# Performance work log

Hardware: AMD Instinct MI355X
Metric: run time of the kernel (lower is better)

Reference implementation:

```python
import jax, jax.numpy as jnp
import numpy as np

B, P, S, D, H = 4, 256, 4096, 1024, 16
HD = D // H
EPS = 1e-5


def setup_inputs() -> dict:
    key = jax.random.key(0)
    ks = jax.random.split(key, 12)
    patch_embeddings = jax.random.normal(ks[0], (B, P, D), dtype=jnp.float32)
    byte_hidden_states = jax.random.normal(ks[1], (B, S, D), dtype=jnp.float32)
    # contiguous non-overlapping spans of 16 bytes per patch
    starts = jnp.broadcast_to(jnp.arange(P, dtype=jnp.int64) * (S // P), (B, P))
    ends = starts + (S // P)
    patch_positions = jnp.stack([starts, ends], axis=-1)  # (B, P, 2)
    byte_mask = jnp.ones((B, S), dtype=jnp.float32)
    scale = 0.02
    return {
        "patch_embeddings": patch_embeddings,
        "byte_hidden_states": byte_hidden_states,
        "patch_positions": patch_positions,
        "byte_mask": byte_mask,
        "ln_gamma": jnp.ones((D,), jnp.float32),
        "ln_beta": jnp.zeros((D,), jnp.float32),
        "w_q": jax.random.normal(ks[2], (D, D), jnp.float32) * scale,
        "b_q": jnp.zeros((D,), jnp.float32),
        "w_k": jax.random.normal(ks[3], (D, D), jnp.float32) * scale,
        "b_k": jnp.zeros((D,), jnp.float32),
        "w_v": jax.random.normal(ks[4], (D, D), jnp.float32) * scale,
        "b_v": jnp.zeros((D,), jnp.float32),
        "w_o": jax.random.normal(ks[5], (D, D), jnp.float32) * scale,
        "b_o": jnp.zeros((D,), jnp.float32),
    }


def _layernorm(x, gamma, beta):
    mu = jnp.mean(x, axis=-1, keepdims=True)
    var = jnp.mean(jnp.square(x - mu), axis=-1, keepdims=True)
    return (x - mu) * jax.lax.rsqrt(var + EPS) * gamma + beta


def reference(patch_embeddings, byte_hidden_states, patch_positions, byte_mask,
              ln_gamma, ln_beta, w_q, b_q, w_k, b_k, w_v, b_v, w_o, b_o):
    b, p, d = patch_embeddings.shape
    s = byte_hidden_states.shape[1]
    h, hd = H, d // H

    start = patch_positions[..., 0]  # (B,P)
    end = patch_positions[..., 1]
    idx = jnp.arange(s)
    valid_span = (start < s) & (end <= s) & (start < end)  # (B,P)
    window = (idx[None, None, :] >= start[..., None]) & (idx[None, None, :] < end[..., None])
    allowed = window & valid_span[..., None]               # (B,P,S) boolean mask
    allowed = allowed & (byte_mask[:, None, :] != 0.0)

    # query from layernormed patch embeddings (1 query per patch)
    qx = _layernorm(patch_embeddings, ln_gamma, ln_beta)
    q = (qx @ w_q.T + b_q).reshape(b, p, h, hd)
    k = (byte_hidden_states @ w_k.T + b_k).reshape(b, s, h, hd)
    v = (byte_hidden_states @ w_v.T + b_v).reshape(b, s, h, hd)

    scale = 1.0 / jnp.sqrt(jnp.asarray(hd, patch_embeddings.dtype))
    scores = jnp.einsum('bphd,bshd->bhps', q, k) * scale      # (B,H,P,S)
    scores = jnp.where(allowed[:, None, :, :], scores, jnp.asarray(-1e9, scores.dtype))
    attn = jax.nn.softmax(scores, axis=-1)
    out = jnp.einsum('bhps,bshd->bphd', attn, v).reshape(b, p, d)
    out = out @ w_o.T + b_o

    # dropout is identity in eval mode; residual add
    return patch_embeddings + out
```

## Files before the change

### kernel.cpp

```cpp
#include <hip/hip_runtime.h>
#include <hip/hip_bf16.h>
#include <stdint.h>

#define B_ 4
#define P_ 256
#define S_ 4096
#define D_ 1024
#define H_ 16
#define HD_ 64

typedef __attribute__((ext_vector_type(8))) short short8;
typedef __attribute__((ext_vector_type(4))) short short4v;
typedef __attribute__((ext_vector_type(2))) short short2v;
typedef __attribute__((ext_vector_type(4))) float f32x4;

__device__ __forceinline__ float b2f(short s) {
  return __uint_as_float(((unsigned)(unsigned short)s) << 16);
}
__device__ __forceinline__ short f2bf(float f) {
  unsigned u = __float_as_uint(f);
  unsigned r = (u + 0x7fffu + ((u >> 16) & 1u)) >> 16;
  return (short)(unsigned short)r;
}

__global__ __launch_bounds__(256) void prep2_kernel(
    const float* __restrict__ pe,
    const float* __restrict__ gamma, const float* __restrict__ beta,
    const float* __restrict__ wq, const float* __restrict__ wk,
    const float* __restrict__ wv, const float* __restrict__ wo,
    short* __restrict__ wqb, short* __restrict__ wvb, short* __restrict__ wob,
    short* __restrict__ wkT, short* __restrict__ qx)
{
  const int bid = blockIdx.x;
  const int tid = threadIdx.x;
  if (bid < 1536) {
    const int wi = bid >> 9;
    const size_t base = (size_t)(bid & 511) * 2048 + (size_t)tid * 8;
    const float* src; short* dst;
    if (wi == 0)      { src = wq; dst = wqb; }
    else if (wi == 1) { src = wv; dst = wvb; }
    else              { src = wo; dst = wob; }
    const float4 f0 = *(const float4*)(src + base);
    const float4 f1 = *(const float4*)(src + base + 4);
    short8 o;
    o[0] = f2bf(f0.x); o[1] = f2bf(f0.y); o[2] = f2bf(f0.z); o[3] = f2bf(f0.w);
    o[4] = f2bf(f1.x); o[5] = f2bf(f1.y); o[6] = f2bf(f1.z); o[7] = f2bf(f1.w);
    *(short8*)(dst + base) = o;
  } else if (bid < 1600) {
    __shared__ short Ts[128][132];
    const int t = bid - 1536;
    const int ti = t >> 3, tj = t & 7;
    #pragma unroll
    for (int j = 0; j < 16; ++j) {
      const int r = j * 8 + (tid >> 5);
      const int c4 = (tid & 31) * 4;
      const float4 v = *(const float4*)(wk + (size_t)(ti * 128 + r) * D_ + tj * 128 + c4);
      short4v o;
      o[0] = f2bf(v.x); o[1] = f2bf(v.y); o[2] = f2bf(v.z); o[3] = f2bf(v.w);
      *(short4v*)(&Ts[r][c4]) = o;
    }
    __syncthreads();
    #pragma unroll
    for (int j = 0; j < 16; ++j) {
      const int c = j * 8 + (tid >> 5);
      const int r4 = (tid & 31) * 4;
      short4v o;
      o[0] = Ts[r4 + 0][c]; o[1] = Ts[r4 + 1][c];
      o[2] = Ts[r4 + 2][c]; o[3] = Ts[r4 + 3][c];
      *(short4v*)(wkT + (size_t)(tj * 128 + c) * D_ + ti * 128 + r4) = o;
    }
  } else {
    const int row = bid - 1600;
    const int c = tid * 4;
    const float4 x = *(const float4*)(pe + (size_t)row * D_ + c);
    float s1 = x.x + x.y + x.z + x.w;
    float s2 = x.x * x.x + x.y * x.y + x.z * x.z + x.w * x.w;
    #pragma unroll
    for (int off = 32; off >= 1; off >>= 1) {
      s1 += __shfl_xor(s1, off, 64);
      s2 += __shfl_xor(s2, off, 64);
    }
    __shared__ float red[8];
    const int wid = tid >> 6, lane = tid & 63;
    if (lane == 0) { red[wid] = s1; red[4 + wid] = s2; }
    __syncthreads();
    s1 = red[0] + red[1] + red[2] + red[3];
    s2 = red[4] + red[5] + red[6] + red[7];
    const float mu = s1 * (1.0f / D_);
    const float var = s2 * (1.0f / D_) - mu * mu;
    const float rs = rsqrtf(var + 1e-5f);
    const float4 g = *(const float4*)(gamma + c);
    const float4 bt = *(const float4*)(beta + c);
    short4v o;
    o[0] = f2bf((x.x - mu) * rs * g.x + bt.x);
    o[1] = f2bf((x.y - mu) * rs * g.y + bt.y);
    o[2] = f2bf((x.z - mu) * rs * g.z + bt.z);
    o[3] = f2bf((x.w - mu) * rs * g.w + bt.w);
    *(short4v*)(qx + (size_t)row * D_ + c) = o;
  }
}

__device__ __forceinline__ void gemm64_core(
    const short* __restrict__ A, const short* __restrict__ W,
    int mt, int nt, int Kd, int lda, int ldb,
    f32x4 acc[2][2], short* As, short* Bs)
{
  const int tid = threadIdx.x;
  const int w = tid >> 6, l = tid & 63;
  const int wr = w >> 1, wc = w & 1;
  const int lr = l & 15, lk = l >> 4;
  (void)l; (void)w;

  for (int kt = 0; kt < Kd; kt += 64) {
    __syncthreads();
    #pragma unroll
    for (int j = 0; j < 2; ++j) {
      const int c = j * 256 + tid;
      const int r = c >> 3;
      const int ce = ((c & 7) ^ (r & 7)) * 8;
      __builtin_amdgcn_global_load_lds(
          (const __attribute__((address_space(1))) void*)(A + (size_t)(mt * 64 + r) * lda + kt + ce),
          (__attribute__((address_space(3))) void*)((char*)As + c * 16), 16, 0, 0);
      __builtin_amdgcn_global_load_lds(
          (const __attribute__((address_space(1))) void*)(W + (size_t)(nt * 64 + r) * ldb + kt + ce),
          (__attribute__((address_space(3))) void*)((char*)Bs + c * 16), 16, 0, 0);
    }
    asm volatile("s_waitcnt vmcnt(0)" ::: "memory");
    __syncthreads();
    #pragma unroll
    for (int ks = 0; ks < 2; ++ks) {
      short8 a[2], bfr[2];
      #pragma unroll
      for (int m = 0; m < 2; ++m) {
        const int row = wr * 32 + m * 16 + lr;
        a[m] = *(const short8*)((char*)As + row * 128 + (((ks * 4 + lk) ^ (row & 7)) * 16));
      }
      #pragma unroll
      for (int n = 0; n < 2; ++n) {
        const int row = wc * 32 + n * 16 + lr;
        bfr[n] = *(const short8*)((char*)Bs + row * 128 + (((ks * 4 + lk) ^ (row & 7)) * 16));
      }
      #pragma unroll
      for (int m = 0; m < 2; ++m)
        #pragma unroll
        for (int n = 0; n < 2; ++n)
          acc[m][n] = __builtin_amdgcn_mfma_f32_16x16x32_bf16(a[m], bfr[n], acc[m][n], 0, 0, 0);
    }
  }
}

__global__ __launch_bounds__(256) void gemm_q64(
    const short* __restrict__ qx, const short* __restrict__ wqb,
    const float* __restrict__ b_q, short* __restrict__ Qo)
{
  __shared__ __align__(16) short As[64 * 64];
  __shared__ __align__(16) short Bs[64 * 64];
  const int bid = blockIdx.x;
  const int u = (bid & 7) * 32 + (bid >> 3);
  const int mt = u >> 4, nt = u & 15;

  f32x4 acc[2][2] = {};
  gemm64_core(qx, wqb, mt, nt, D_, D_, D_, acc, As, Bs);

  const int l = threadIdx.x & 63, w = threadIdx.x >> 6;
  const int wr = w >> 1, wc = w & 1;
  const int lr = l & 15, lk = l >> 4;
  #pragma unroll
  for (int n = 0; n < 2; ++n) {
    const int col = nt * 64 + wc * 32 + n * 16 + lr;
    const float bv = b_q[col];
    #pragma unroll
    for (int m = 0; m < 2; ++m) {
      const int row0 = mt * 64 + wr * 32 + m * 16 + lk * 4;
      #pragma unroll
      for (int i = 0; i < 4; ++i)
        Qo[(size_t)(row0 + i) * D_ + col] = f2bf(acc[m][n][i] + bv);
    }
  }
}

__global__ __launch_bounds__(256) void gemm_qt(
    const short* __restrict__ Qo, const short* __restrict__ wkT,
    short* __restrict__ Qt)
{
  __shared__ __align__(16) short As[128 * 64];
  __shared__ __align__(16) short Bs[128 * 64];
  const int bid = blockIdx.x;
  const int hh = bid >> 6, mt = (bid >> 3) & 7, nt = bid & 7;
  const int tid = threadIdx.x;
  const int wid = tid >> 6, l = tid & 63;
  const int wr = wid >> 1, wc = wid & 1;
  const int lr = l & 15, lk = l >> 4;
  const int sr = l >> 3, scol = (l & 7) * 8;

  #pragma unroll
  for (int j = 0; j < 4; ++j) {
    const int r = (wid * 4 + j) * 8 + sr;
    __builtin_amdgcn_global_load_lds(
        (const __attribute__((address_space(1))) void*)(Qo + (size_t)(mt * 128 + r) * D_ + hh * 64 + scol),
        (__attribute__((address_space(3))) void*)(As + (wid * 4 + j) * 512), 16, 0, 0);
    __builtin_amdgcn_global_load_lds(
        (const __attribute__((address_space(1))) void*)(wkT + (size_t)(nt * 128 + r) * D_ + hh * 64 + scol),
        (__attribute__((address_space(3))) void*)(Bs + (wid * 4 + j) * 512), 16, 0, 0);
  }
  asm volatile("s_waitcnt vmcnt(0)" ::: "memory");
  __syncthreads();

  f32x4 acc[4][4] = {};
  #pragma unroll
  for (int ks = 0; ks < 2; ++ks) {
    short8 a[4], bfr[4];
    #pragma unroll
    for (int m = 0; m < 4; ++m)
      a[m] = *(const short8*)(As + (wr * 64 + m * 16 + lr) * 64 + ks * 32 + lk * 8);
    #pragma unroll
    for (int n = 0; n < 4; ++n)
      bfr[n] = *(const short8*)(Bs + (wc * 64 + n * 16 + lr) * 64 + ks * 32 + lk * 8);
    #pragma unroll
    for (int m = 0; m < 4; ++m)
      #pragma unroll
      for (int n = 0; n < 4; ++n)
        acc[m][n] = __builtin_amdgcn_mfma_f32_16x16x32_bf16(a[m], bfr[n], acc[m][n], 0, 0, 0);
  }

  #pragma unroll
  for (int n = 0; n < 4; ++n) {
    const int col = nt * 128 + wc * 64 + n * 16 + lr;
    #pragma unroll
    for (int m = 0; m < 4; ++m) {
      const int row0 = mt * 128 + wr * 64 + m * 16 + lk * 4;
      #pragma unroll
      for (int i = 0; i < 4; ++i)
        Qt[((size_t)(row0 + i) * 16 + hh) * D_ + col] = f2bf(acc[m][n][i]);
    }
  }
}

__global__ __launch_bounds__(512) void attn2_kernel(
    const short* __restrict__ Qt, const float* __restrict__ X,
    const int* __restrict__ pos, const float* __restrict__ mask,
    short* __restrict__ Xbar)
{
  __shared__ __align__(16) short Xs[16 * 1024];
  __shared__ float attnT[16][16];
  __shared__ float rband[16];
  __shared__ float denL[16];
  __shared__ __align__(16) float red[8][256];

  const int bp = blockIdx.x;
  const int b = bp >> 8;
  const int tid = threadIdx.x;
  const int w = tid >> 6, l = tid & 63;
  const int t_l = l & 15;
  const int lk = l >> 4;
  const int hgrp = lk * 4;

  short8 af[4];
  {
    const short* qb = Qt + ((size_t)bp * 16 + t_l) * D_;
    #pragma unroll
    for (int ks = 0; ks < 4; ++ks)
      af[ks] = *(const short8*)(qb + (w * 4 + ks) * 32 + lk * 8);
  }

  const bool is64 = (pos[1] == 0);
  const int start = is64 ? pos[4 * bp]     : pos[2 * bp];
  const int end   = is64 ? pos[4 * bp + 2] : pos[2 * bp + 1];
  const bool valid = (start < S_) && (end <= S_) && (start < end);
  const int lo = valid ? (start < 0 ? 0 : start) : 0;
  const int hi = valid ? end : 0;

  float xacc[16][2];
  #pragma unroll
  for (int h = 0; h < 16; ++h) { xacc[h][0] = 0.f; xacc[h][1] = 0.f; }
  float m_run[4] = {-3.0e38f, -3.0e38f, -3.0e38f, -3.0e38f};
  float den[4] = {0.f, 0.f, 0.f, 0.f};

  for (int c0 = lo; c0 < hi; c0 += 16) {
    __syncthreads();
    #pragma unroll
    for (int j = 0; j < 16; ++j) {
      int rg = c0 + j; rg = rg < S_ ? rg : S_ - 1;
      const float2 xv = *(const float2*)(X + ((size_t)b * S_ + rg) * D_ + tid * 2);
      short2v o;
      o[0] = f2bf(xv.x); o[1] = f2bf(xv.y);
      *(short2v*)((char*)Xs + j * 2048 + ((tid * 4) ^ ((j & 7) << 4))) = o;
    }
    __syncthreads();

    f32x4 c = {};
    const int rsw = (t_l & 7) << 4;
    #pragma unroll
    for (int ks = 0; ks < 4; ++ks) {
      const int kb = ((w * 4 + ks) * 32 + lk * 8) * 2;
      const short8 x8 = *(const short8*)((char*)Xs + t_l * 2048 + (kb ^ rsw));
      c = __builtin_amdgcn_mfma_f32_16x16x32_bf16(af[ks], x8, c, 0, 0, 0);
    }
    *(f32x4*)&red[w][l * 4] = c;
    __syncthreads();
    f32x4 s = *(const f32x4*)&red[0][l * 4];
    #pragma unroll
    for (int ww = 1; ww < 8; ++ww)
      s = s + *(const f32x4*)&red[ww][l * 4];

    const int tg = c0 + t_l;
    const bool ok = (tg < hi) && (mask[(size_t)b * S_ + tg] != 0.f);
    float wgt[4], rr[4];
    #pragma unroll
    for (int i = 0; i < 4; ++i) {
      const float sc = ok ? s[i] * 0.125f : -3.0e38f;
      float cm = sc;
      cm = fmaxf(cm, __shfl_xor(cm, 1, 64));
      cm = fmaxf(cm, __shfl_xor(cm, 2, 64));
      cm = fmaxf(cm, __shfl_xor(cm, 4, 64));
      cm = fmaxf(cm, __shfl_xor(cm, 8, 64));
      const float nm = fmaxf(m_run[i], cm);
      const float r = __expf(m_run[i] - nm);
      const float wv_ = ok ? __expf(sc - nm) : 0.f;
      float ws = wv_;
      ws += __shfl_xor(ws, 1, 64);
      ws += __shfl_xor(ws, 2, 64);
      ws += __shfl_xor(ws, 4, 64);
      ws += __shfl_xor(ws, 8, 64);
      den[i] = den[i] * r + ws;
      m_run[i] = nm;
      wgt[i] = wv_; rr[i] = r;
    }
    if (w == 0) {
      #pragma unroll
      for (int i = 0; i < 4; ++i) attnT[t_l][hgrp + i] = wgt[i];
      if (t_l == 0) {
        #pragma unroll
        for (int i = 0; i < 4; ++i) rband[hgrp + i] = rr[i];
      }
    }
    __syncthreads();

    #pragma unroll
    for (int h = 0; h < 16; ++h) {
      const float rb = rband[h];
      xacc[h][0] *= rb; xacc[h][1] *= rb;
    }
    #pragma unroll
    for (int t = 0; t < 16; ++t) {
      const f32x4 a0 = *(const f32x4*)&attnT[t][0];
      const f32x4 a1 = *(const f32x4*)&attnT[t][4];
      const f32x4 a2 = *(const f32x4*)&attnT[t][8];
      const f32x4 a3 = *(const f32x4*)&attnT[t][12];
      const short2v xv = *(const short2v*)((char*)Xs + t * 2048 + ((tid * 4) ^ ((t & 7) << 4)));
      const float x0 = b2f(xv[0]), x1 = b2f(xv[1]);
      #pragma unroll
      for (int i = 0; i < 4; ++i) {
        xacc[i][0]      += a0[i] * x0; xacc[i][1]      += a0[i] * x1;
        xacc[i + 4][0]  += a1[i] * x0; xacc[i + 4][1]  += a1[i] * x1;
        xacc[i + 8][0]  += a2[i] * x0; xacc[i + 8][1]  += a2[i] * x1;
        xacc[i + 12][0] += a3[i] * x0; xacc[i + 12][1] += a3[i] * x1;
      }
    }
  }

  if (w == 0 && t_l == 0) {
    #pragma unroll
    for (int i = 0; i < 4; ++i) denL[hgrp + i] = den[i];
  }
  __syncthreads();

  bool need = false;
  #pragma unroll
  for (int h = 0; h < 16; ++h) need = need || (denL[h] <= 0.f);
  float ms[2] = {0.f, 0.f};
  if (need) {
    for (int t = 0; t < S_; ++t) {
      const float2 xv = *(const float2*)(X + ((size_t)b * S_ + t) * D_ + tid * 2);
      ms[0] += xv.x; ms[1] += xv.y;
    }
    ms[0] *= (1.f / S_); ms[1] *= (1.f / S_);
  }
  #pragma unroll
  for (int h = 0; h < 16; ++h) {
    const float dL = denL[h];
    short2v o;
    if (dL > 0.f) {
      const float inv = 1.f / dL;
      o[0] = f2bf(xacc[h][0] * inv); o[1] = f2bf(xacc[h][1] * inv);
    } else {
      o[0] = f2bf(ms[0]); o[1] = f2bf(ms[1]);
    }
    *(short2v*)(Xbar + ((size_t)bp * 16 + h) * D_ + tid * 2) = o;
  }
}

__global__ __launch_bounds__(256) void gemm_v64(
    const short* __restrict__ Xbar, const short* __restrict__ wvb,
    const float* __restrict__ b_v, short* __restrict__ AO)
{
  __shared__ __align__(16) short As[64 * 64];
  __shared__ __align__(16) short Bs[64 * 64];
  const int bid = blockIdx.x;
  const int u = (bid & 7) * 32 + (bid >> 3);
  const int h = u >> 4, mt = u & 15;

  f32x4 acc[2][2] = {};
  gemm64_core(Xbar + (size_t)h * D_, wvb + (size_t)h * 64 * D_,
              mt, 0, D_, 16 * D_, D_, acc, As, Bs);

  const int l = threadIdx.x & 63, w = threadIdx.x >> 6;
  const int wr = w >> 1, wc = w & 1;
  const int lr = l & 15, lk = l >> 4;
  #pragma unroll
  for (int n = 0; n < 2; ++n) {
    const int gcol = h * 64 + wc * 32 + n * 16 + lr;
    const float bv = b_v[gcol];
    #pragma unroll
    for (int m = 0; m < 2; ++m) {
      const int row0 = mt * 64 + wr * 32 + m * 16 + lk * 4;
      #pragma unroll
      for (int i = 0; i < 4; ++i)
        AO[(size_t)(row0 + i) * D_ + gcol] = f2bf(acc[m][n][i] + bv);
    }
  }
}

__global__ __launch_bounds__(256) void gemm_o64(
    const short* __restrict__ AO, const short* __restrict__ wob,
    const float* __restrict__ b_o, const float* __restrict__ pe,
    float* __restrict__ out)
{
  __shared__ __align__(16) short As[64 * 64];
  __shared__ __align__(16) short Bs[64 * 64];
  const int bid = blockIdx.x;
  const int u = (bid & 7) * 32 + (bid >> 3);
  const int mt = u >> 4, nt = u & 15;

  f32x4 acc[2][2] = {};
  gemm64_core(AO, wob, mt, nt, D_, D_, D_, acc, As, Bs);

  const int l = threadIdx.x & 63, w = threadIdx.x >> 6;
  const int wr = w >> 1, wc = w & 1;
  const int lr = l & 15, lk = l >> 4;
  #pragma unroll
  for (int n = 0; n < 2; ++n) {
    const int col = nt * 64 + wc * 32 + n * 16 + lr;
    const float bv = b_o[col];
    #pragma unroll
    for (int m = 0; m < 2; ++m) {
      const int row0 = mt * 64 + wr * 32 + m * 16 + lk * 4;
      #pragma unroll
      for (int i = 0; i < 4; ++i) {
        const size_t idx = (size_t)(row0 + i) * D_ + col;
        out[idx] = acc[m][n][i] + bv + pe[idx];
      }
    }
  }
}

extern "C" void kernel_launch(void* const* d_in, const int* in_sizes, int n_in,
                              void* d_out, int out_size, void* d_ws, size_t ws_size,
                              hipStream_t stream)
{
  const float* pe    = (const float*)d_in[0];
  const float* xby   = (const float*)d_in[1];
  const int*   pos   = (const int*)d_in[2];
  const float* mask  = (const float*)d_in[3];
  const float* gamma = (const float*)d_in[4];
  const float* beta  = (const float*)d_in[5];
  const float* w_q   = (const float*)d_in[6];
  const float* b_q   = (const float*)d_in[7];
  const float* w_k   = (const float*)d_in[8];
  const float* b_k   = (const float*)d_in[9];  (void)b_k;
  const float* w_v   = (const float*)d_in[10];
  const float* b_v   = (const float*)d_in[11];
  const float* w_o   = (const float*)d_in[12];
  const float* b_o   = (const float*)d_in[13];

  char* ws = (char*)d_ws;
  short* Qt   = (short*)(ws);
  short* Xbar = (short*)(ws + 33554432);
  short* wqb  = (short*)(ws + 67108864);
  short* wvb  = (short*)(ws + 69206016);
  short* wob  = (short*)(ws + 71303168);
  short* wkT  = (short*)(ws + 73400320);
  short* qx   = (short*)(ws + 75497472);
  short* Qo   = (short*)(ws + 77594624);
  short* AO   = (short*)(ws + 79691776);
  (void)in_sizes; (void)n_in; (void)out_size; (void)ws_size;

  prep2_kernel<<<2624, 256, 0, stream>>>(pe, gamma, beta, w_q, w_k, w_v, w_o,
                                         wqb, wvb, wob, wkT, qx);
  gemm_q64<<<256, 256, 0, stream>>>(qx, wqb, b_q, Qo);
  gemm_qt<<<1024, 256, 0, stream>>>(Qo, wkT, Qt);
  attn2_kernel<<<1024, 512, 0, stream>>>(Qt, xby, pos, mask, Xbar);
  gemm_v64<<<256, 256, 0, stream>>>(Xbar, wvb, b_v, AO);
  gemm_o64<<<256, 256, 0, stream>>>(AO, wob, b_o, pe, (float*)d_out);
}
```

Baseline: 101.2 us.

## Process four patches per attention block with register-prefetched next span

The attention kernel now handles four consecutive patches per block (256 blocks instead of 1024). While one patch is computed, the next patch's first 16 byte rows and its query fragments are prefetched into registers, then written to shared memory. The aim is to hide global load latency behind compute. In exchange there are fewer blocks to fill the GPU (256 blocks on a 256-CU part), more register pressure from the prefetch buffer, and no effect for spans longer than 16 beyond the first chunk.

```diff
diff --git a/kernel.cpp b/kernel.cpp
--- a/kernel.cpp
+++ b/kernel.cpp
@@ -236,7 +236,7 @@
   }
 }
 
-__global__ __launch_bounds__(512) void attn2_kernel(
+__global__ __launch_bounds__(512) void attn5_kernel(
     const short* __restrict__ Qt, const float* __restrict__ X,
     const int* __restrict__ pos, const float* __restrict__ mask,
     short* __restrict__ Xbar)
@@ -247,147 +247,199 @@
   __shared__ float denL[16];
   __shared__ __align__(16) float red[8][256];
 
-  const int bp = blockIdx.x;
-  const int b = bp >> 8;
+  const int bp0 = blockIdx.x * 4;
+  const int b = bp0 >> 8;
   const int tid = threadIdx.x;
   const int w = tid >> 6, l = tid & 63;
-  const int t_l = l & 15;
-  const int lk = l >> 4;
+  const int t_l = l & 15, lk = l >> 4;
   const int hgrp = lk * 4;
 
-  short8 af[4];
-  {
-    const short* qb = Qt + ((size_t)bp * 16 + t_l) * D_;
-    #pragma unroll
-    for (int ks = 0; ks < 4; ++ks)
-      af[ks] = *(const short8*)(qb + (w * 4 + ks) * 32 + lk * 8);
-  }
-
   const bool is64 = (pos[1] == 0);
-  const int start = is64 ? pos[4 * bp]     : pos[2 * bp];
-  const int end   = is64 ? pos[4 * bp + 2] : pos[2 * bp + 1];
-  const bool valid = (start < S_) && (end <= S_) && (start < end);
-  const int lo = valid ? (start < 0 ? 0 : start) : 0;
-  const int hi = valid ? end : 0;
-
-  float xacc[16][2];
-  #pragma unroll
-  for (int h = 0; h < 16; ++h) { xacc[h][0] = 0.f; xacc[h][1] = 0.f; }
-  float m_run[4] = {-3.0e38f, -3.0e38f, -3.0e38f, -3.0e38f};
-  float den[4] = {0.f, 0.f, 0.f, 0.f};
-
-  for (int c0 = lo; c0 < hi; c0 += 16) {
+  int plo[4], phi[4];
+  #pragma unroll
+  for (int p = 0; p < 4; ++p) {
+    const int bp = bp0 + p;
+    const int st = is64 ? pos[4 * bp]     : pos[2 * bp];
+    const int en = is64 ? pos[4 * bp + 2] : pos[2 * bp + 1];
+    const bool v = (st < S_) && (en <= S_) && (st < en);
+    plo[p] = v ? (st < 0 ? 0 : st) : 0;
+    phi[p] = v ? en : 0;
+  }
+
+  float2 pre[16];
+  auto XPRE = [&](int p) {
+    #pragma unroll
+    for (int j = 0; j < 16; ++j) {
+      int rg = plo[p] + j; rg = rg < S_ ? rg : S_ - 1;
+      pre[j] = *(const float2*)(X + ((size_t)b * S_ + rg) * D_ + tid * 2);
+    }
+  };
+  auto XWRITE = [&]() {
+    #pragma unroll
+    for (int j = 0; j < 16; ++j) {
+      short2v o; o[0] = f2bf(pre[j].x); o[1] = f2bf(pre[j].y);
+      *(short2v*)((char*)Xs + j * 2048 + ((tid * 4) ^ ((j & 7) << 4))) = o;
+    }
+  };
+
+  short8 af0[4], af1[4];
+#define LOADAF(arr, bp_)                                                     \
+  {                                                                          \
+    const short* qb_ = Qt + ((size_t)(bp_) * 16 + t_l) * D_;                 \
+    _Pragma("unroll")                                                        \
+    for (int ks = 0; ks < 4; ++ks)                                           \
+      arr[ks] = *(const short8*)(qb_ + (w * 4 + ks) * 32 + lk * 8);          \
+  }
+
+  auto DO_PATCH = [&](const short8 (&af)[4], int p) {
+    const int lo = plo[p], hi = phi[p];
+    const int bp = bp0 + p;
+    float xacc[16][2];
+    #pragma unroll
+    for (int h = 0; h < 16; ++h) { xacc[h][0] = 0.f; xacc[h][1] = 0.f; }
+    float m_run[4] = {-3.0e38f, -3.0e38f, -3.0e38f, -3.0e38f};
+    float den[4] = {0.f, 0.f, 0.f, 0.f};
+
+    bool first = true;
+    for (int c0 = lo; c0 < hi; c0 += 16) {
+      if (!first) {
+        __syncthreads();
+        #pragma unroll
+        for (int j = 0; j < 16; ++j) {
+          int rg = c0 + j; rg = rg < S_ ? rg : S_ - 1;
+          const float2 xv = *(const float2*)(X + ((size_t)b * S_ + rg) * D_ + tid * 2);
+          short2v o; o[0] = f2bf(xv.x); o[1] = f2bf(xv.y);
+          *(short2v*)((char*)Xs + j * 2048 + ((tid * 4) ^ ((j & 7) << 4))) = o;
+        }
+        __syncthreads();
+      }
+      first = false;
+
+      f32x4 c = {};
+      const int rsw = (t_l & 7) << 4;
+      #pragma unroll
+      for (int ks = 0; ks < 4; ++ks) {
+        const int kb = ((w * 4 + ks) * 32 + lk * 8) * 2;
+        const short8 x8 = *(const short8*)((char*)Xs + t_l * 2048 + (kb ^ rsw));
+        c = __builtin_amdgcn_mfma_f32_16x16x32_bf16(af[ks], x8, c, 0, 0, 0);
+      }
+      *(f32x4*)&red[w][l * 4] = c;
+      __syncthreads();
+      f32x4 s = *(const f32x4*)&red[0][l * 4];
+      #pragma unroll
+      for (int ww = 1; ww < 8; ++ww)
+        s = s + *(const f32x4*)&red[ww][l * 4];
+
+      const int tg = c0 + t_l;
+      const bool ok = (tg < hi) && (mask[(size_t)b * S_ + tg] != 0.f);
+      float wgt[4], rr[4];
+      #pragma unroll
+      for (int i = 0; i < 4; ++i) {
+        const float sc = ok ? s[i] * 0.125f : -3.0e38f;
+        float cm = sc;
+        cm = fmaxf(cm, __shfl_xor(cm, 1, 64));
+        cm = fmaxf(cm, __shfl_xor(cm, 2, 64));
+        cm = fmaxf(cm, __shfl_xor(cm, 4, 64));
+        cm = fmaxf(cm, __shfl_xor(cm, 8, 64));
+        const float nm = fmaxf(m_run[i], cm);
+        const float r = __expf(m_run[i] - nm);
+        const float wv_ = ok ? __expf(sc - nm) : 0.f;
+        float ws = wv_;
+        ws += __shfl_xor(ws, 1, 64);
+        ws += __shfl_xor(ws, 2, 64);
+        ws += __shfl_xor(ws, 4, 64);
+        ws += __shfl_xor(ws, 8, 64);
+        den[i] = den[i] * r + ws;
+        m_run[i] = nm;
+        wgt[i] = wv_; rr[i] = r;
+      }
+      if (w == 0) {
+        #pragma unroll
+        for (int i = 0; i < 4; ++i) attnT[t_l][hgrp + i] = wgt[i];
+        if (t_l == 0) {
+          #pragma unroll
+          for (int i = 0; i < 4; ++i) rband[hgrp + i] = rr[i];
+        }
+      }
+      __syncthreads();
+
+      #pragma unroll
+      for (int h = 0; h < 16; ++h) {
+        const float rb = rband[h];
+        xacc[h][0] *= rb; xacc[h][1] *= rb;
+      }
+      #pragma unroll
+      for (int t = 0; t < 16; ++t) {
+        const f32x4 a0 = *(const f32x4*)&attnT[t][0];
+        const f32x4 a1 = *(const f32x4*)&attnT[t][4];
+        const f32x4 a2 = *(const f32x4*)&attnT[t][8];
+        const f32x4 a3 = *(const f32x4*)&attnT[t][12];
+        const short2v xv = *(const short2v*)((char*)Xs + t * 2048 + ((tid * 4) ^ ((t & 7) << 4)));
+        const float x0 = b2f(xv[0]), x1 = b2f(xv[1]);
+        #pragma unroll
+        for (int i = 0; i < 4; ++i) {
+          xacc[i][0]      += a0[i] * x0; xacc[i][1]      += a0[i] * x1;
+          xacc[i + 4][0]  += a1[i] * x0; xacc[i + 4][1]  += a1[i] * x1;
+          xacc[i + 8][0]  += a2[i] * x0; xacc[i + 8][1]  += a2[i] * x1;
+          xacc[i + 12][0] += a3[i] * x0; xacc[i + 12][1] += a3[i] * x1;
+        }
+      }
+    }
+
+    if (w == 0 && t_l == 0) {
+      #pragma unroll
+      for (int i = 0; i < 4; ++i) denL[hgrp + i] = den[i];
+    }
     __syncthreads();
-    #pragma unroll
-    for (int j = 0; j < 16; ++j) {
-      int rg = c0 + j; rg = rg < S_ ? rg : S_ - 1;
-      const float2 xv = *(const float2*)(X + ((size_t)b * S_ + rg) * D_ + tid * 2);
+
+    bool need = false;
+    #pragma unroll
+    for (int h = 0; h < 16; ++h) need = need || (denL[h] <= 0.f);
+    float ms[2] = {0.f, 0.f};
+    if (need) {
+      for (int t = 0; t < S_; ++t) {
+        const float2 xv = *(const float2*)(X + ((size_t)b * S_ + t) * D_ + tid * 2);
+        ms[0] += xv.x; ms[1] += xv.y;
+      }
+      ms[0] *= (1.f / S_); ms[1] *= (1.f / S_);
+    }
+    #pragma unroll
+    for (int h = 0; h < 16; ++h) {
+      const float dL = denL[h];
       short2v o;
-      o[0] = f2bf(xv.x); o[1] = f2bf(xv.y);
-      *(short2v*)((char*)Xs + j * 2048 + ((tid * 4) ^ ((j & 7) << 4))) = o;
-    }
-    __syncthreads();
-
-    f32x4 c = {};
-    const int rsw = (t_l & 7) << 4;
-    #pragma unroll
-    for (int ks = 0; ks < 4; ++ks) {
-      const int kb = ((w * 4 + ks) * 32 + lk * 8) * 2;
-      const short8 x8 = *(const short8*)((char*)Xs + t_l * 2048 + (kb ^ rsw));
-      c = __builtin_amdgcn_mfma_f32_16x16x32_bf16(af[ks], x8, c, 0, 0, 0);
-    }
-    *(f32x4*)&red[w][l * 4] = c;
-    __syncthreads();
-    f32x4 s = *(const f32x4*)&red[0][l * 4];
-    #pragma unroll
-    for (int ww = 1; ww < 8; ++ww)
-      s = s + *(const f32x4*)&red[ww][l * 4];
-
-    const int tg = c0 + t_l;
-    const bool ok = (tg < hi) && (mask[(size_t)b * S_ + tg] != 0.f);
-    float wgt[4], rr[4];
-    #pragma unroll
-    for (int i = 0; i < 4; ++i) {
-      const float sc = ok ? s[i] * 0.125f : -3.0e38f;
-      float cm = sc;
-      cm = fmaxf(cm, __shfl_xor(cm, 1, 64));
-      cm = fmaxf(cm, __shfl_xor(cm, 2, 64));
-      cm = fmaxf(cm, __shfl_xor(cm, 4, 64));
-      cm = fmaxf(cm, __shfl_xor(cm, 8, 64));
-      const float nm = fmaxf(m_run[i], cm);
-      const float r = __expf(m_run[i] - nm);
-      const float wv_ = ok ? __expf(sc - nm) : 0.f;
-      float ws = wv_;
-      ws += __shfl_xor(ws, 1, 64);
-      ws += __shfl_xor(ws, 2, 64);
-      ws += __shfl_xor(ws, 4, 64);
-      ws += __shfl_xor(ws, 8, 64);
-      den[i] = den[i] * r + ws;
-      m_run[i] = nm;
-      wgt[i] = wv_; rr[i] = r;
-    }
-    if (w == 0) {
-      #pragma unroll
-      for (int i = 0; i < 4; ++i) attnT[t_l][hgrp + i] = wgt[i];
-      if (t_l == 0) {
-        #pragma unroll
-        for (int i = 0; i < 4; ++i) rband[hgrp + i] = rr[i];
-      }
-    }
-    __syncthreads();
-
-    #pragma unroll
-    for (int h = 0; h < 16; ++h) {
-      const float rb = rband[h];
-      xacc[h][0] *= rb; xacc[h][1] *= rb;
-    }
-    #pragma unroll
-    for (int t = 0; t < 16; ++t) {
-      const f32x4 a0 = *(const f32x4*)&attnT[t][0];
-      const f32x4 a1 = *(const f32x4*)&attnT[t][4];
-      const f32x4 a2 = *(const f32x4*)&attnT[t][8];
-      const f32x4 a3 = *(const f32x4*)&attnT[t][12];
-      const short2v xv = *(const short2v*)((char*)Xs + t * 2048 + ((tid * 4) ^ ((t & 7) << 4)));
-      const float x0 = b2f(xv[0]), x1 = b2f(xv[1]);
-      #pragma unroll
-      for (int i = 0; i < 4; ++i) {
-        xacc[i][0]      += a0[i] * x0; xacc[i][1]      += a0[i] * x1;
-        xacc[i + 4][0]  += a1[i] * x0; xacc[i + 4][1]  += a1[i] * x1;
-        xacc[i + 8][0]  += a2[i] * x0; xacc[i + 8][1]  += a2[i] * x1;
-        xacc[i + 12][0] += a3[i] * x0; xacc[i + 12][1] += a3[i] * x1;
-      }
-    }
-  }
-
-  if (w == 0 && t_l == 0) {
-    #pragma unroll
-    for (int i = 0; i < 4; ++i) denL[hgrp + i] = den[i];
-  }
-  __syncthreads();
-
-  bool need = false;
-  #pragma unroll
-  for (int h = 0; h < 16; ++h) need = need || (denL[h] <= 0.f);
-  float ms[2] = {0.f, 0.f};
-  if (need) {
-    for (int t = 0; t < S_; ++t) {
-      const float2 xv = *(const float2*)(X + ((size_t)b * S_ + t) * D_ + tid * 2);
-      ms[0] += xv.x; ms[1] += xv.y;
-    }
-    ms[0] *= (1.f / S_); ms[1] *= (1.f / S_);
-  }
-  #pragma unroll
-  for (int h = 0; h < 16; ++h) {
-    const float dL = denL[h];
-    short2v o;
-    if (dL > 0.f) {
-      const float inv = 1.f / dL;
-      o[0] = f2bf(xacc[h][0] * inv); o[1] = f2bf(xacc[h][1] * inv);
-    } else {
-      o[0] = f2bf(ms[0]); o[1] = f2bf(ms[1]);
-    }
-    *(short2v*)(Xbar + ((size_t)bp * 16 + h) * D_ + tid * 2) = o;
-  }
+      if (dL > 0.f) {
+        const float inv = 1.f / dL;
+        o[0] = f2bf(xacc[h][0] * inv); o[1] = f2bf(xacc[h][1] * inv);
+      } else {
+        o[0] = f2bf(ms[0]); o[1] = f2bf(ms[1]);
+      }
+      *(short2v*)(Xbar + ((size_t)bp * 16 + h) * D_ + tid * 2) = o;
+    }
+  };
+
+  XPRE(0); LOADAF(af0, bp0 + 0);
+
+  XWRITE();
+  __syncthreads();
+  XPRE(1); LOADAF(af1, bp0 + 1);
+  DO_PATCH(af0, 0);
+
+  __syncthreads();
+  XWRITE();
+  __syncthreads();
+  XPRE(2); LOADAF(af0, bp0 + 2);
+  DO_PATCH(af1, 1);
+
+  __syncthreads();
+  XWRITE();
+  __syncthreads();
+  XPRE(3); LOADAF(af1, bp0 + 3);
+  DO_PATCH(af0, 2);
+
+  __syncthreads();
+  XWRITE();
+  __syncthreads();
+  DO_PATCH(af1, 3);
 }
 
 __global__ __launch_bounds__(256) void gemm_v64(
@@ -489,7 +541,7 @@
                                          wqb, wvb, wob, wkT, qx);
   gemm_q64<<<256, 256, 0, stream>>>(qx, wqb, b_q, Qo);
   gemm_qt<<<1024, 256, 0, stream>>>(Qo, wkT, Qt);
-  attn2_kernel<<<1024, 512, 0, stream>>>(Qt, xby, pos, mask, Xbar);
+  attn5_kernel<<<256, 512, 0, stream>>>(Qt, xby, pos, mask, Xbar);
   gemm_v64<<<256, 256, 0, stream>>>(Xbar, wvb, b_v, AO);
   gemm_o64<<<256, 256, 0, stream>>>(AO, wob, b_o, pe, (float*)d_out);
 }
```

Result: slower. 155.0 us (+53.2%).

## Pre-convert byte states to bf16 and double-buffer async LDS loads in attention

Applied to the files above, without the earlier changes.

The prep kernel now also converts the full byte hidden-state tensor to bf16 in workspace. The attention kernel processes two patches per block and uses global_load_lds directly into a double-buffered shared tile, so staging of the second patch overlaps compute on the first. This is meant to cut global read bandwidth and hide load latency in attention. The cost is an extra full pass over the 64MB fp32 input plus a 32MB bf16 write in prep, and half as many attention blocks.

```diff
diff --git a/kernel.cpp b/kernel.cpp
--- a/kernel.cpp
+++ b/kernel.cpp
@@ -23,19 +23,28 @@
   return (short)(unsigned short)r;
 }
 
-__global__ __launch_bounds__(256) void prep2_kernel(
-    const float* __restrict__ pe,
+__global__ __launch_bounds__(256) void prep3_kernel(
+    const float* __restrict__ xbytes, const float* __restrict__ pe,
     const float* __restrict__ gamma, const float* __restrict__ beta,
     const float* __restrict__ wq, const float* __restrict__ wk,
     const float* __restrict__ wv, const float* __restrict__ wo,
-    short* __restrict__ wqb, short* __restrict__ wvb, short* __restrict__ wob,
-    short* __restrict__ wkT, short* __restrict__ qx)
+    short* __restrict__ Xb, short* __restrict__ wqb, short* __restrict__ wvb,
+    short* __restrict__ wob, short* __restrict__ wkT, short* __restrict__ qx)
 {
   const int bid = blockIdx.x;
   const int tid = threadIdx.x;
-  if (bid < 1536) {
-    const int wi = bid >> 9;
-    const size_t base = (size_t)(bid & 511) * 2048 + (size_t)tid * 8;
+  if (bid < 8192) {
+    const size_t base = (size_t)bid * 2048 + (size_t)tid * 8;
+    const float4 f0 = *(const float4*)(xbytes + base);
+    const float4 f1 = *(const float4*)(xbytes + base + 4);
+    short8 o;
+    o[0] = f2bf(f0.x); o[1] = f2bf(f0.y); o[2] = f2bf(f0.z); o[3] = f2bf(f0.w);
+    o[4] = f2bf(f1.x); o[5] = f2bf(f1.y); o[6] = f2bf(f1.z); o[7] = f2bf(f1.w);
+    *(short8*)(Xb + base) = o;
+  } else if (bid < 9728) {
+    const int r = bid - 8192;
+    const int wi = r >> 9;
+    const size_t base = (size_t)(r & 511) * 2048 + (size_t)tid * 8;
     const float* src; short* dst;
     if (wi == 0)      { src = wq; dst = wqb; }
     else if (wi == 1) { src = wv; dst = wvb; }
@@ -46,9 +55,9 @@
     o[0] = f2bf(f0.x); o[1] = f2bf(f0.y); o[2] = f2bf(f0.z); o[3] = f2bf(f0.w);
     o[4] = f2bf(f1.x); o[5] = f2bf(f1.y); o[6] = f2bf(f1.z); o[7] = f2bf(f1.w);
     *(short8*)(dst + base) = o;
-  } else if (bid < 1600) {
+  } else if (bid < 9792) {
     __shared__ short Ts[128][132];
-    const int t = bid - 1536;
+    const int t = bid - 9728;
     const int ti = t >> 3, tj = t & 7;
     #pragma unroll
     for (int j = 0; j < 16; ++j) {
@@ -70,7 +79,7 @@
       *(short4v*)(wkT + (size_t)(tj * 128 + c) * D_ + ti * 128 + r4) = o;
     }
   } else {
-    const int row = bid - 1600;
+    const int row = bid - 9792;
     const int c = tid * 4;
     const float4 x = *(const float4*)(pe + (size_t)row * D_ + c);
     float s1 = x.x + x.y + x.z + x.w;
@@ -236,158 +245,191 @@
   }
 }
 
-__global__ __launch_bounds__(512) void attn2_kernel(
-    const short* __restrict__ Qt, const float* __restrict__ X,
+__global__ __launch_bounds__(512) void attn6_kernel(
+    const short* __restrict__ Qt, const short* __restrict__ Xb,
     const int* __restrict__ pos, const float* __restrict__ mask,
     short* __restrict__ Xbar)
 {
-  __shared__ __align__(16) short Xs[16 * 1024];
+  __shared__ __align__(16) short Xs[2][16 * 1024];
   __shared__ float attnT[16][16];
   __shared__ float rband[16];
   __shared__ float denL[16];
   __shared__ __align__(16) float red[8][256];
 
-  const int bp = blockIdx.x;
-  const int b = bp >> 8;
+  const int bp0 = blockIdx.x * 2;
+  const int b = bp0 >> 8;
   const int tid = threadIdx.x;
   const int w = tid >> 6, l = tid & 63;
-  const int t_l = l & 15;
-  const int lk = l >> 4;
+  const int t_l = l & 15, lk = l >> 4;
   const int hgrp = lk * 4;
 
-  short8 af[4];
-  {
-    const short* qb = Qt + ((size_t)bp * 16 + t_l) * D_;
-    #pragma unroll
-    for (int ks = 0; ks < 4; ++ks)
-      af[ks] = *(const short8*)(qb + (w * 4 + ks) * 32 + lk * 8);
-  }
-
   const bool is64 = (pos[1] == 0);
-  const int start = is64 ? pos[4 * bp]     : pos[2 * bp];
-  const int end   = is64 ? pos[4 * bp + 2] : pos[2 * bp + 1];
-  const bool valid = (start < S_) && (end <= S_) && (start < end);
-  const int lo = valid ? (start < 0 ? 0 : start) : 0;
-  const int hi = valid ? end : 0;
-
-  float xacc[16][2];
-  #pragma unroll
-  for (int h = 0; h < 16; ++h) { xacc[h][0] = 0.f; xacc[h][1] = 0.f; }
-  float m_run[4] = {-3.0e38f, -3.0e38f, -3.0e38f, -3.0e38f};
-  float den[4] = {0.f, 0.f, 0.f, 0.f};
-
-  for (int c0 = lo; c0 < hi; c0 += 16) {
+  int plo[2], phi[2];
+  #pragma unroll
+  for (int p = 0; p < 2; ++p) {
+    const int bp = bp0 + p;
+    const int st = is64 ? pos[4 * bp]     : pos[2 * bp];
+    const int en = is64 ? pos[4 * bp + 2] : pos[2 * bp + 1];
+    const bool v = (st < S_) && (en <= S_) && (st < en);
+    plo[p] = v ? (st < 0 ? 0 : st) : 0;
+    phi[p] = v ? en : 0;
+  }
+
+  auto STAGE = [&](int buf, int c0) {
+    #pragma unroll
+    for (int jj = 0; jj < 4; ++jj) {
+      const int seg = w * 4 + jj;
+      const int row = seg >> 1, half = seg & 1;
+      int rg = c0 + row; rg = rg < S_ ? rg : S_ - 1;
+      const int src = (half * 1024 + l * 16) ^ ((row & 7) << 4);
+      __builtin_amdgcn_global_load_lds(
+          (const __attribute__((address_space(1))) void*)((const char*)(Xb + (size_t)(b * S_ + rg) * D_) + src),
+          (__attribute__((address_space(3))) void*)((char*)Xs + buf * 32768 + row * 2048 + half * 1024 + l * 16),
+          16, 0, 0);
+    }
+  };
+
+  auto DO_PATCH = [&](int buf, int p) {
+    const int lo = plo[p], hi = phi[p];
+    const int bp = bp0 + p;
+    const char* Xbuf = (const char*)Xs + buf * 32768;
+
+    float xacc[16][2];
+    #pragma unroll
+    for (int h = 0; h < 16; ++h) { xacc[h][0] = 0.f; xacc[h][1] = 0.f; }
+    float m_run[4] = {-3.0e38f, -3.0e38f, -3.0e38f, -3.0e38f};
+    float den[4] = {0.f, 0.f, 0.f, 0.f};
+
+    short8 af[4];
+    {
+      const short* qb = Qt + ((size_t)bp * 16 + t_l) * D_;
+      #pragma unroll
+      for (int ks = 0; ks < 4; ++ks)
+        af[ks] = *(const short8*)(qb + (w * 4 + ks) * 32 + lk * 8);
+    }
+
+    bool first = true;
+    for (int c0 = lo; c0 < hi; c0 += 16) {
+      if (!first) {
+        __syncthreads();
+        STAGE(buf, c0);
+        asm volatile("s_waitcnt vmcnt(0)" ::: "memory");
+        __syncthreads();
+      }
+      first = false;
+
+      f32x4 c = {};
+      const int rsw = (t_l & 7) << 4;
+      #pragma unroll
+      for (int ks = 0; ks < 4; ++ks) {
+        const int kb = ((w * 4 + ks) * 32 + lk * 8) * 2;
+        const short8 x8 = *(const short8*)(Xbuf + t_l * 2048 + (kb ^ rsw));
+        c = __builtin_amdgcn_mfma_f32_16x16x32_bf16(af[ks], x8, c, 0, 0, 0);
+      }
+      *(f32x4*)&red[w][l * 4] = c;
+      __syncthreads();
+      f32x4 s = *(const f32x4*)&red[0][l * 4];
+      #pragma unroll
+      for (int ww = 1; ww < 8; ++ww)
+        s = s + *(const f32x4*)&red[ww][l * 4];
+
+      const int tg = c0 + t_l;
+      const bool ok = (tg < hi) && (mask[(size_t)b * S_ + tg] != 0.f);
+      float wgt[4], rr[4];
+      #pragma unroll
+      for (int i = 0; i < 4; ++i) {
+        const float sc = ok ? s[i] * 0.125f : -3.0e38f;
+        float cm = sc;
+        cm = fmaxf(cm, __shfl_xor(cm, 1, 64));
+        cm = fmaxf(cm, __shfl_xor(cm, 2, 64));
+        cm = fmaxf(cm, __shfl_xor(cm, 4, 64));
+        cm = fmaxf(cm, __shfl_xor(cm, 8, 64));
+        const float nm = fmaxf(m_run[i], cm);
+        const float r = __expf(m_run[i] - nm);
+        const float wv_ = ok ? __expf(sc - nm) : 0.f;
+        float ws = wv_;
+        ws += __shfl_xor(ws, 1, 64);
+        ws += __shfl_xor(ws, 2, 64);
+        ws += __shfl_xor(ws, 4, 64);
+        ws += __shfl_xor(ws, 8, 64);
+        den[i] = den[i] * r + ws;
+        m_run[i] = nm;
+        wgt[i] = wv_; rr[i] = r;
+      }
+      if (w == 0) {
+        #pragma unroll
+        for (int i = 0; i < 4; ++i) attnT[t_l][hgrp + i] = wgt[i];
+        if (t_l == 0) {
+          #pragma unroll
+          for (int i = 0; i < 4; ++i) rband[hgrp + i] = rr[i];
+        }
+      }
+      __syncthreads();
+
+      #pragma unroll
+      for (int h = 0; h < 16; ++h) {
+        const float rb = rband[h];
+        xacc[h][0] *= rb; xacc[h][1] *= rb;
+      }
+      #pragma unroll
+      for (int t = 0; t < 16; ++t) {
+        const f32x4 a0 = *(const f32x4*)&attnT[t][0];
+        const f32x4 a1 = *(const f32x4*)&attnT[t][4];
+        const f32x4 a2 = *(const f32x4*)&attnT[t][8];
+        const f32x4 a3 = *(const f32x4*)&attnT[t][12];
+        const short2v xv = *(const short2v*)(Xbuf + t * 2048 + ((tid * 4) ^ ((t & 7) << 4)));
+        const float x0 = b2f(xv[0]), x1 = b2f(xv[1]);
+        #pragma unroll
+        for (int i = 0; i < 4; ++i) {
+          xacc[i][0]      += a0[i] * x0; xacc[i][1]      += a0[i] * x1;
+          xacc[i + 4][0]  += a1[i] * x0; xacc[i + 4][1]  += a1[i] * x1;
+          xacc[i + 8][0]  += a2[i] * x0; xacc[i + 8][1]  += a2[i] * x1;
+          xacc[i + 12][0] += a3[i] * x0; xacc[i + 12][1] += a3[i] * x1;
+        }
+      }
+    }
+
+    if (w == 0 && t_l == 0) {
+      #pragma unroll
+      for (int i = 0; i < 4; ++i) denL[hgrp + i] = den[i];
+    }
     __syncthreads();
-    #pragma unroll
-    for (int j = 0; j < 16; ++j) {
-      int rg = c0 + j; rg = rg < S_ ? rg : S_ - 1;
-      const float2 xv = *(const float2*)(X + ((size_t)b * S_ + rg) * D_ + tid * 2);
+
+    bool need = false;
+    #pragma unroll
+    for (int h = 0; h < 16; ++h) need = need || (denL[h] <= 0.f);
+    float ms[2] = {0.f, 0.f};
+    if (need) {
+      for (int t = 0; t < S_; ++t) {
+        const short2v xv = *(const short2v*)(Xb + ((size_t)b * S_ + t) * D_ + tid * 2);
+        ms[0] += b2f(xv[0]); ms[1] += b2f(xv[1]);
+      }
+      ms[0] *= (1.f / S_); ms[1] *= (1.f / S_);
+    }
+    #pragma unroll
+    for (int h = 0; h < 16; ++h) {
+      const float dL = denL[h];
       short2v o;
-      o[0] = f2bf(xv.x); o[1] = f2bf(xv.y);
-      *(short2v*)((char*)Xs + j * 2048 + ((tid * 4) ^ ((j & 7) << 4))) = o;
-    }
-    __syncthreads();
-
-    f32x4 c = {};
-    const int rsw = (t_l & 7) << 4;
-    #pragma unroll
-    for (int ks = 0; ks < 4; ++ks) {
-      const int kb = ((w * 4 + ks) * 32 + lk * 8) * 2;
-      const short8 x8 = *(const short8*)((char*)Xs + t_l * 2048 + (kb ^ rsw));
-      c = __builtin_amdgcn_mfma_f32_16x16x32_bf16(af[ks], x8, c, 0, 0, 0);
-    }
-    *(f32x4*)&red[w][l * 4] = c;
-    __syncthreads();
-    f32x4 s = *(const f32x4*)&red[0][l * 4];
-    #pragma unroll
-    for (int ww = 1; ww < 8; ++ww)
-      s = s + *(const f32x4*)&red[ww][l * 4];
-
-    const int tg = c0 + t_l;
-    const bool ok = (tg < hi) && (mask[(size_t)b * S_ + tg] != 0.f);
-    float wgt[4], rr[4];
-    #pragma unroll
-    for (int i = 0; i < 4; ++i) {
-      const float sc = ok ? s[i] * 0.125f : -3.0e38f;
-      float cm = sc;
-      cm = fmaxf(cm, __shfl_xor(cm, 1, 64));
-      cm = fmaxf(cm, __shfl_xor(cm, 2, 64));
-      cm = fmaxf(cm, __shfl_xor(cm, 4, 64));
-      cm = fmaxf(cm, __shfl_xor(cm, 8, 64));
-      const float nm = fmaxf(m_run[i], cm);
-      const float r = __expf(m_run[i] - nm);
-      const float wv_ = ok ? __expf(sc - nm) : 0.f;
-      float ws = wv_;
-      ws += __shfl_xor(ws, 1, 64);
-      ws += __shfl_xor(ws, 2, 64);
-      ws += __shfl_xor(ws, 4, 64);
-      ws += __shfl_xor(ws, 8, 64);
-      den[i] = den[i] * r + ws;
-      m_run[i] = nm;
-      wgt[i] = wv_; rr[i] = r;
-    }
-    if (w == 0) {
-      #pragma unroll
-      for (int i = 0; i < 4; ++i) attnT[t_l][hgrp + i] = wgt[i];
-      if (t_l == 0) {
-        #pragma unroll
-        for (int i = 0; i < 4; ++i) rband[hgrp + i] = rr[i];
-      }
-    }
-    __syncthreads();
-
-    #pragma unroll
-    for (int h = 0; h < 16; ++h) {
-      const float rb = rband[h];
-      xacc[h][0] *= rb; xacc[h][1] *= rb;
-    }
-    #pragma unroll
-    for (int t = 0; t < 16; ++t) {
-      const f32x4 a0 = *(const f32x4*)&attnT[t][0];
-      const f32x4 a1 = *(const f32x4*)&attnT[t][4];
-      const f32x4 a2 = *(const f32x4*)&attnT[t][8];
-      const f32x4 a3 = *(const f32x4*)&attnT[t][12];
-      const short2v xv = *(const short2v*)((char*)Xs + t * 2048 + ((tid * 4) ^ ((t & 7) << 4)));
-      const float x0 = b2f(xv[0]), x1 = b2f(xv[1]);
-      #pragma unroll
-      for (int i = 0; i < 4; ++i) {
-        xacc[i][0]      += a0[i] * x0; xacc[i][1]      += a0[i] * x1;
-        xacc[i + 4][0]  += a1[i] * x0; xacc[i + 4][1]  += a1[i] * x1;
-        xacc[i + 8][0]  += a2[i] * x0; xacc[i + 8][1]  += a2[i] * x1;
-        xacc[i + 12][0] += a3[i] * x0; xacc[i + 12][1] += a3[i] * x1;
-      }
-    }
-  }
-
-  if (w == 0 && t_l == 0) {
-    #pragma unroll
-    for (int i = 0; i < 4; ++i) denL[hgrp + i] = den[i];
-  }
+      if (dL > 0.f) {
+        const float inv = 1.f / dL;
+        o[0] = f2bf(xacc[h][0] * inv); o[1] = f2bf(xacc[h][1] * inv);
+      } else {
+        o[0] = f2bf(ms[0]); o[1] = f2bf(ms[1]);
+      }
+      *(short2v*)(Xbar + ((size_t)bp * 16 + h) * D_ + tid * 2) = o;
+    }
+  };
+
+  STAGE(0, plo[0]);
+  asm volatile("s_waitcnt vmcnt(0)" ::: "memory");
   __syncthreads();
 
-  bool need = false;
-  #pragma unroll
-  for (int h = 0; h < 16; ++h) need = need || (denL[h] <= 0.f);
-  float ms[2] = {0.f, 0.f};
-  if (need) {
-    for (int t = 0; t < S_; ++t) {
-      const float2 xv = *(const float2*)(X + ((size_t)b * S_ + t) * D_ + tid * 2);
-      ms[0] += xv.x; ms[1] += xv.y;
-    }
-    ms[0] *= (1.f / S_); ms[1] *= (1.f / S_);
-  }
-  #pragma unroll
-  for (int h = 0; h < 16; ++h) {
-    const float dL = denL[h];
-    short2v o;
-    if (dL > 0.f) {
-      const float inv = 1.f / dL;
-      o[0] = f2bf(xacc[h][0] * inv); o[1] = f2bf(xacc[h][1] * inv);
-    } else {
-      o[0] = f2bf(ms[0]); o[1] = f2bf(ms[1]);
-    }
-    *(short2v*)(Xbar + ((size_t)bp * 16 + h) * D_ + tid * 2) = o;
-  }
+  STAGE(1, plo[1]);
+  DO_PATCH(0, 0);
+  asm volatile("s_waitcnt vmcnt(0)" ::: "memory");
+  __syncthreads();
+
+  DO_PATCH(1, 1);
 }
 
 __global__ __launch_bounds__(256) void gemm_v64(
@@ -483,13 +525,14 @@
   short* qx   = (short*)(ws + 75497472);
   short* Qo   = (short*)(ws + 77594624);
   short* AO   = (short*)(ws + 79691776);
+  short* Xb   = (short*)(ws + 81788928);
   (void)in_sizes; (void)n_in; (void)out_size; (void)ws_size;
 
-  prep2_kernel<<<2624, 256, 0, stream>>>(pe, gamma, beta, w_q, w_k, w_v, w_o,
-                                         wqb, wvb, wob, wkT, qx);
+  prep3_kernel<<<10816, 256, 0, stream>>>(xby, pe, gamma, beta, w_q, w_k, w_v, w_o,
+                                          Xb, wqb, wvb, wob, wkT, qx);
   gemm_q64<<<256, 256, 0, stream>>>(qx, wqb, b_q, Qo);
   gemm_qt<<<1024, 256, 0, stream>>>(Qo, wkT, Qt);
-  attn2_kernel<<<1024, 512, 0, stream>>>(Qt, xby, pos, mask, Xbar);
+  attn6_kernel<<<512, 512, 0, stream>>>(Qt, Xb, pos, mask, Xbar);
   gemm_v64<<<256, 256, 0, stream>>>(Xbar, wvb, b_v, AO);
   gemm_o64<<<256, 256, 0, stream>>>(AO, wob, b_o, pe, (float*)d_out);
 }
```

Result: slower. 112.1 us (+10.8%).
